# Performance work log

Measured on AMD Instinct MI355X. Metric: run time of the kernel, lower is better.

## Reference

```python
import jax, jax.numpy as jnp
import numpy as np

N, E, B = 25000, 400000, 64          # nodes, edges, graphs
F, ED, H, C = 32, 8, 4, 32           # feature/edge dims, heads, per-head dim
HC = H * C
L = 4                                # init conv + 3 stacked convs (same shapes)
LIN = 128


def setup_inputs() -> dict:
    key = jax.random.key(0)
    ks = jax.random.split(key, 24)
    s = 0.05
    inp = {
        "x": jax.random.normal(ks[0], (N, F), jnp.float32),
        "edge_attr": jax.random.normal(ks[1], (E, ED), jnp.float32),
        "edge_index": jax.random.randint(ks[2], (2, E), 0, N),
        "batch_index": jnp.sort(jax.random.randint(ks[3], (N,), 0, B)),
        # stacked TransformerConv params (leading dim = layer)
        "Wq": jax.random.normal(ks[4], (L, F, HC), jnp.float32) * s,
        "bq": jnp.zeros((L, HC), jnp.float32),
        "Wk": jax.random.normal(ks[5], (L, F, HC), jnp.float32) * s,
        "bk": jnp.zeros((L, HC), jnp.float32),
        "Wv": jax.random.normal(ks[6], (L, F, HC), jnp.float32) * s,
        "bv": jnp.zeros((L, HC), jnp.float32),
        "We": jax.random.normal(ks[7], (L, ED, HC), jnp.float32) * s,
        "be": jnp.zeros((L, HC), jnp.float32),
        "Wskip": jax.random.normal(ks[8], (L, F, HC), jnp.float32) * s,
        "bskip": jnp.zeros((L, HC), jnp.float32),
        "Wbeta": jax.random.normal(ks[9], (L, 3 * HC, 1), jnp.float32) * s,
        # per-layer Linear(H*C -> emb) + BatchNorm
        "Wlin": jax.random.normal(ks[10], (L, HC, F), jnp.float32) * s,
        "blin": jnp.zeros((L, F), jnp.float32),
        "bn_gamma": jnp.ones((L, F), jnp.float32),
        "bn_beta": jnp.zeros((L, F), jnp.float32),
        # readout MLP
        "W1": jax.random.normal(ks[11], (2 * F, LIN), jnp.float32) * s,
        "b1": jnp.zeros((LIN,), jnp.float32),
        "W2": jax.random.normal(ks[12], (LIN, LIN // 2), jnp.float32) * s,
        "b2": jnp.zeros((LIN // 2,), jnp.float32),
        "W3": jax.random.normal(ks[13], (LIN // 2, 1), jnp.float32) * s,
        "b3": jnp.zeros((1,), jnp.float32),
    }
    return inp


def _transformer_conv(x, edge_attr, src, dst, Wq, bq, Wk, bk, Wv, bv, We, be,
                      Wskip, bskip, Wbeta):
    """PyG TransformerConv(heads=H, concat=True, beta=True, edge_dim=ED), eval mode."""
    n = x.shape[0]
    q = (x @ Wq + bq).reshape(n, H, C)
    k = (x @ Wk + bk).reshape(n, H, C)
    v = (x @ Wv + bv).reshape(n, H, C)
    e = (edge_attr @ We + be).reshape(-1, H, C)          # [E,H,C]
    kj = k[src] + e                                       # key_j + edge
    alpha = jnp.einsum('ehc,ehc->eh', q[dst], kj) / np.sqrt(C).astype(np.float32)
    # segment softmax over incoming edges per destination node
    amax = jax.ops.segment_max(alpha, dst, num_segments=n)
    a = jnp.exp(alpha - amax[dst])
    denom = jax.ops.segment_sum(a, dst, num_segments=n)
    a = a / denom[dst]                                    # [E,H]
    msg = (v[src] + e) * a[:, :, None]
    out = jax.ops.segment_sum(msg, dst, num_segments=n).reshape(n, HC)
    x_skip = x @ Wskip + bskip
    beta = jax.nn.sigmoid(
        jnp.concatenate([out, x_skip, out - x_skip], axis=-1) @ Wbeta)  # [N,1]
    return beta * x_skip + (1.0 - beta) * out


def _bn(h, gamma, beta):
    m = h.mean(axis=0)
    v = h.var(axis=0)
    return (h - m) * jax.lax.rsqrt(v + 1e-5) * gamma + beta


def reference(x, edge_attr, edge_index, batch_index,
              Wq, bq, Wk, bk, Wv, bv, We, be, Wskip, bskip, Wbeta,
              Wlin, blin, bn_gamma, bn_beta, W1, b1, W2, b2, W3, b3):
    src, dst = edge_index[0], edge_index[1]
    counts = jax.ops.segment_sum(jnp.ones((N,), jnp.float32), batch_index,
                                 num_segments=B)[:, None]
    h = x
    rep = jnp.zeros((B, 2 * F), jnp.float32)
    for i in range(L):
        h = _transformer_conv(h, edge_attr, src, dst,
                              Wq[i], bq[i], Wk[i], bk[i], Wv[i], bv[i],
                              We[i], be[i], Wskip[i], bskip[i], Wbeta[i])
        h = jax.nn.elu(h @ Wlin[i] + blin[i])
        h = _bn(h, bn_gamma[i], bn_beta[i])
        if i > 0:  # original pools only inside the n_layers loop
            gmx = jax.ops.segment_max(h, batch_index, num_segments=B)
            gmean = jax.ops.segment_sum(h, batch_index, num_segments=B) / counts
            rep = rep + jnp.concatenate([gmx, gmean], axis=1)
    z = jax.nn.elu(rep @ W1 + b1)
    z = jax.nn.elu(z @ W2 + b2)
    return z @ W3 + b3  # [B,1]
```

## Files before the change

kernel.cpp:

```cpp
#include <hip/hip_runtime.h>
#include <hip/hip_bf16.h>
#include <hip/hip_fp16.h>
#include <math.h>

#define NN 25000
#define EE 400000
#define BB 64
#define FF 32
#define EDD 8
#define HH 4
#define CC 32
#define HCC 128
#define LL 4
#define LINN 128

#define RSQRT_C 0.17677669529663687f
#define NREP 16
#define NREPP 8
#define GMAX_OFF (NREP * 64)
#define GSUM_OFF (NREP * 64 + NREPP * BB * 32)
#define LSTATS_WORDS (NREP * 64 + 2 * NREPP * BB * 32)


__global__ void deg_kernel(const int* __restrict__ dst, int* __restrict__ deg) {
    int i = blockIdx.x * blockDim.x + threadIdx.x;
    if (i < EE) atomicAdd(&deg[dst[i]], 1);
}

__global__ void scan1_kernel(const int* __restrict__ deg, int* __restrict__ rowp, int* __restrict__ blks) {
    __shared__ int s[256];
    int i = blockIdx.x * 256 + threadIdx.x;
    int v = (i < NN) ? deg[i] : 0;
    s[threadIdx.x] = v;
    __syncthreads();
    for (int off = 1; off < 256; off <<= 1) {
        int t = (threadIdx.x >= off) ? s[threadIdx.x - off] : 0;
        __syncthreads();
        s[threadIdx.x] += t;
        __syncthreads();
    }
    if (i < NN) rowp[i + 1] = s[threadIdx.x];
    if (threadIdx.x == 255) blks[blockIdx.x] = s[255];
    if (i == 0) rowp[0] = 0;
}

__global__ void scan2_kernel(int* __restrict__ blks, int nb,
                             const int* __restrict__ bidx, int* __restrict__ gstart) {
    __shared__ int s[128];
    int t = threadIdx.x;
    int v = (t < nb) ? blks[t] : 0;
    s[t] = v;
    __syncthreads();
    for (int off = 1; off < 128; off <<= 1) {
        int u = (t >= off) ? s[t - off] : 0;
        __syncthreads();
        s[t] += u;
        __syncthreads();
    }
    if (t < nb) blks[t] = s[t] - v;
    if (t <= BB) {
        int lo = 0, hi = NN;
        while (lo < hi) { int mid = (lo + hi) >> 1; if (bidx[mid] < t) lo = mid + 1; else hi = mid; }
        gstart[t] = lo;
    }
}

__global__ void scan3_kernel(int* __restrict__ rowp, const int* __restrict__ blks) {
    int i = blockIdx.x * 256 + threadIdx.x;
    if (i < NN) rowp[i + 1] += blks[blockIdx.x];
}

__global__ void fill_kernel(const int* __restrict__ dst, const int* __restrict__ rowp,
                            int* __restrict__ cnt2, int* __restrict__ eid) {
    int i = blockIdx.x * blockDim.x + threadIdx.x;
    if (i < EE) {
        int d = dst[i];
        int pos = rowp[d] + atomicAdd(&cnt2[d], 1);
        eid[pos] = i;
    }
}

__global__ void sortseg_kernel(const int* __restrict__ rowp, int* __restrict__ eid) {
    int n = blockIdx.x * 256 + threadIdx.x;
    if (n >= NN) return;
    int b = rowp[n], e = rowp[n + 1];
    int d = e - b;
    if (d <= 1) return;
    if (d <= 64) {
        int buf[64];
        for (int i = 0; i < d; ++i) buf[i] = eid[b + i];
        for (int i = 1; i < d; ++i) {
            int key = buf[i];
            int j = i - 1;
            while (j >= 0 && buf[j] > key) { buf[j + 1] = buf[j]; --j; }
            buf[j + 1] = key;
        }
        for (int i = 0; i < d; ++i) eid[b + i] = buf[i];
    } else {
        for (int i = b + 1; i < e; ++i) {
            int key = eid[i];
            int j = i - 1;
            while (j >= b && eid[j] > key) { eid[j + 1] = eid[j]; --j; }
            eid[j + 1] = key;
        }
    }
}

__global__ void csr_gather_kernel(const int* __restrict__ csre, const int* __restrict__ srcA,
                                  const float* __restrict__ eattr,
                                  int* __restrict__ csrsrc, uint4* __restrict__ eh) {
    int j = blockIdx.x * blockDim.x + threadIdx.x;
    if (j < EE) {
        int e = csre[j];
        csrsrc[j] = srcA[e];
        const float4* s = (const float4*)(eattr + (size_t)e * 8);
        float4 s0 = s[0], s1 = s[1];
        __half2 h0 = __float22half2_rn(make_float2(s0.x, s0.y));
        __half2 h1 = __float22half2_rn(make_float2(s0.z, s0.w));
        __half2 h2 = __float22half2_rn(make_float2(s1.x, s1.y));
        __half2 h3 = __float22half2_rn(make_float2(s1.z, s1.w));
        uint4 o;
        o.x = *(unsigned*)&h0; o.y = *(unsigned*)&h1;
        o.z = *(unsigned*)&h2; o.w = *(unsigned*)&h3;
        eh[j] = o;
    }
}

__global__ __launch_bounds__(256) void qkvs_kernel(
    const float* __restrict__ hin, int applyBN, const float* __restrict__ bnss,
    const float* __restrict__ Wq, const float* __restrict__ bq,
    const float* __restrict__ Wk, const float* __restrict__ bk,
    const float* __restrict__ Wv, const float* __restrict__ bv,
    const float* __restrict__ Ws, const float* __restrict__ bs,
    __half2* __restrict__ qo, __half2* __restrict__ kvo,
    __half2* __restrict__ so, float* __restrict__ lstats)
{
    if (blockIdx.x == 0) {
        for (int i = threadIdx.x; i < LSTATS_WORDS; i += 256) lstats[i] = 0.0f;
    }
    __shared__ float xs[32][32];
    __shared__ float sbns[64];
    if (threadIdx.x < 64) sbns[threadIdx.x] = applyBN ? bnss[threadIdx.x] : (threadIdx.x < 32 ? 1.0f : 0.0f);
    int lane = threadIdx.x & 63;
    int sel = threadIdx.x >> 6;
    const float* W = (sel == 0) ? Wq : (sel == 1) ? Wk : (sel == 2) ? Wv : Ws;
    const float* bias = (sel == 0) ? bq : (sel == 1) ? bk : (sel == 2) ? bv : bs;
    float w0[32], w1[32];
#pragma unroll
    for (int f = 0; f < 32; ++f) {
        float2 t = *(const float2*)&W[f * 128 + 2 * lane];
        w0[f] = t.x; w1[f] = t.y;
    }
    float2 bvv = *(const float2*)&bias[2 * lane];

    int c = lane >> 1;
    int pr = lane & 1;
    int h2k = c * 4 + pr;
    int h2v = c * 4 + 2 + pr;

    for (int chunk = blockIdx.x * 32; chunk < NN; chunk += gridDim.x * 32) {
        __syncthreads();
        for (int i = threadIdx.x; i < 1024; i += 256) {
            int nn = chunk + (i >> 5);
            int ch = i & 31;
            float v = (nn < NN) ? hin[nn * 32 + ch] : 0.0f;
            xs[i >> 5][ch] = v * sbns[ch] + sbns[32 + ch];
        }
        __syncthreads();
        int nmax = NN - chunk; if (nmax > 32) nmax = 32;
        for (int nl = 0; nl < nmax; ++nl) {
            float a0 = bvv.x, a1 = bvv.y;
#pragma unroll
            for (int f = 0; f < 32; ++f) {
                float xv = xs[nl][f];
                a0 += xv * w0[f];
                a1 += xv * w1[f];
            }
            size_t node = (size_t)(chunk + nl);
            __half2 hv = __float22half2_rn(make_float2(a0, a1));
            if (sel == 0)      qo[node * 64 + lane] = hv;
            else if (sel == 1) kvo[node * 128 + h2k] = hv;
            else if (sel == 2) kvo[node * 128 + h2v] = hv;
            else               so[node * 64 + lane] = hv;
        }
    }
}

__device__ __forceinline__ unsigned fmap_u(float x) {
    unsigned u = __float_as_uint(x);
    return (u & 0x80000000u) ? ~u : (u | 0x80000000u);
}
__device__ __forceinline__ float funmap_u(unsigned u) {
    unsigned b = (u & 0x80000000u) ? (u & 0x7fffffffu) : ~u;
    return __uint_as_float(b);
}

__global__ __launch_bounds__(256) void attn_kernel(
    const uint2* __restrict__ qh, const uint4* __restrict__ kvb4,
    const uint2* __restrict__ skh,
    const uint4* __restrict__ eh,
    const int* __restrict__ srcArr,
    const int* __restrict__ rowp,
    const int* __restrict__ bidx,
    const float* __restrict__ WeL, const float* __restrict__ beL,
    const float* __restrict__ WbL,
    const float* __restrict__ WlinL, const float* __restrict__ blinL,
    float* __restrict__ hlin, float* __restrict__ lstats,
    int doPool, int doWriteH)
{
    __shared__ __align__(16) float shc[4 * 128];
    __shared__ float sbn[64];

    int tid = threadIdx.x;
    if (tid < 64) sbn[tid] = 0.0f;
    __syncthreads();

    int w = tid >> 6;
    int lane = tid & 63;
    int n = blockIdx.x * 4 + w;

    if (n < NN) {
        int c = lane & 31;
        int h = lane >> 5;

        float4 we[8];
#pragma unroll
        for (int d = 0; d < 8; ++d) we[d] = *(const float4*)&WeL[d * 128 + 4 * c];
        float4 be4 = *(const float4*)&beL[4 * c];

        uint2 qraw = qh[(size_t)n * 32 + c];
        float2 q01 = __half22float2(*(const __half2*)&qraw.x);
        float2 q23 = __half22float2(*(const __half2*)&qraw.y);
        float4 q4 = make_float4(q01.x * RSQRT_C, q01.y * RSQRT_C,
                                q23.x * RSQRT_C, q23.y * RSQRT_C);

        int beg = rowp[n], end = rowp[n + 1];
        int cnt = end - beg;
        int last = end - 1;

        float s = 0.0f, a0 = 0.0f, a1 = 0.0f, a2 = 0.0f, a3 = 0.0f;

        uint4 kvA = make_uint4(0u, 0u, 0u, 0u), kvB = kvA;
        uint4 eaA = kvA, eaB = kvA;
        int snC = 0, snD = 0;

        if (cnt > 0) {
            int j0 = beg + h;     j0 = (j0 < end) ? j0 : last;
            int j1 = beg + 2 + h; j1 = (j1 < end) ? j1 : last;
            int j2 = beg + 4 + h; j2 = (j2 < end) ? j2 : last;
            int j3 = beg + 6 + h; j3 = (j3 < end) ? j3 : last;
            int snA = srcArr[j0];
            int snB = srcArr[j1];
            snC = srcArr[j2];
            snD = srcArr[j3];
            kvA = kvb4[(size_t)snA * 32 + c];
            kvB = kvb4[(size_t)snB * 32 + c];
            eaA = eh[j0];
            eaB = eh[j1];
        }

        for (int jb = beg; jb < end; jb += 2) {
            int j = jb + h;
            uint4 kvC = kvb4[(size_t)snC * 32 + c];
            int jn = (j + 4 < end) ? j + 4 : last;
            uint4 eaC = eh[jn];
            int j8 = (j + 8 < end) ? j + 8 : last;
            int snE = srcArr[j8];

            float2 e01 = __half22float2(*(const __half2*)&eaA.x);
            float2 e23 = __half22float2(*(const __half2*)&eaA.y);
            float2 e45 = __half22float2(*(const __half2*)&eaA.z);
            float2 e67 = __half22float2(*(const __half2*)&eaA.w);
            float ead[8] = { e01.x, e01.y, e23.x, e23.y, e45.x, e45.y, e67.x, e67.y };

            float ex = be4.x, ey = be4.y, ez = be4.z, ew = be4.w;
#pragma unroll
            for (int d = 0; d < 8; ++d) {
                ex = fmaf(ead[d], we[d].x, ex);
                ey = fmaf(ead[d], we[d].y, ey);
                ez = fmaf(ead[d], we[d].z, ez);
                ew = fmaf(ead[d], we[d].w, ew);
            }

            float2 k01 = __half22float2(*(const __half2*)&kvA.x);
            float2 k23 = __half22float2(*(const __half2*)&kvA.y);
            float2 v01 = __half22float2(*(const __half2*)&kvA.z);
            float2 v23 = __half22float2(*(const __half2*)&kvA.w);

            float p = q4.x * (k01.x + ex) + q4.y * (k01.y + ey)
                    + q4.z * (k23.x + ez) + q4.w * (k23.y + ew);
            p += __shfl_xor(p, 1);
            p += __shfl_xor(p, 2);
            p += __shfl_xor(p, 4);
            float wg = (j < end) ? __expf(p) : 0.0f;
            s += wg;
            a0 = fmaf(wg, v01.x + ex, a0);
            a1 = fmaf(wg, v01.y + ey, a1);
            a2 = fmaf(wg, v23.x + ez, a2);
            a3 = fmaf(wg, v23.y + ew, a3);

            kvA = kvB; kvB = kvC;
            eaA = eaB; eaB = eaC;
            snC = snD; snD = snE;
        }

        s  += __shfl_xor(s, 32);
        a0 += __shfl_xor(a0, 32);
        a1 += __shfl_xor(a1, 32);
        a2 += __shfl_xor(a2, 32);
        a3 += __shfl_xor(a3, 32);

        float rs = (cnt > 0) ? (1.0f / s) : 0.0f;
        float o0 = a0 * rs, o1 = a1 * rs, o2 = a2 * rs, o3 = a3 * rs;

        uint2 skraw = skh[(size_t)n * 32 + c];
        float2 s01 = __half22float2(*(const __half2*)&skraw.x);
        float2 s23 = __half22float2(*(const __half2*)&skraw.y);
        float4 sk4 = make_float4(s01.x, s01.y, s23.x, s23.y);

        float4 wbo = *(const float4*)&WbL[4 * c];
        float4 wbs = *(const float4*)&WbL[128 + 4 * c];
        float4 wbd = *(const float4*)&WbL[256 + 4 * c];

        float t = o0 * wbo.x + sk4.x * wbs.x + (o0 - sk4.x) * wbd.x
                + o1 * wbo.y + sk4.y * wbs.y + (o1 - sk4.y) * wbd.y
                + o2 * wbo.z + sk4.z * wbs.z + (o2 - sk4.z) * wbd.z
                + o3 * wbo.w + sk4.w * wbs.w + (o3 - sk4.w) * wbd.w;
#pragma unroll
        for (int off = 1; off <= 16; off <<= 1) t += __shfl_xor(t, off);
        float beta = 1.0f / (1.0f + __expf(-t));
        float4 hc4;
        hc4.x = beta * sk4.x + (1.0f - beta) * o0;
        hc4.y = beta * sk4.y + (1.0f - beta) * o1;
        hc4.z = beta * sk4.z + (1.0f - beta) * o2;
        hc4.w = beta * sk4.w + (1.0f - beta) * o3;
        if (h == 0) ((float4*)shc)[w * 32 + c] = hc4;
        int cc = lane & 31;
        int half = lane >> 5;
        float acc = 0.0f;
#pragma unroll 8
        for (int i = 0; i < 64; ++i) {
            int ch = half * 64 + i;
            acc += shc[w * 128 + ch] * WlinL[ch * 32 + cc];
        }
        acc += __shfl_xor(acc, 32);
        if (lane < 32) {
            float hv = acc + blinL[lane];
            hv = (hv > 0.0f) ? hv : expm1f(hv);
            if (doWriteH) hlin[n * 32 + lane] = hv;
            atomicAdd(&sbn[lane], hv);
            atomicAdd(&sbn[32 + lane], hv * hv);
            if (doPool) {
                int g = bidx[n];
                int repv = blockIdx.x & (NREPP - 1);
                size_t idx = ((size_t)repv * BB + g) * 32 + lane;
                atomicMax((unsigned*)lstats + GMAX_OFF + idx, fmap_u(hv));
                atomicAdd(lstats + GSUM_OFF + idx, hv);
            }
        }
    }
    __syncthreads();
    if (tid < 64) atomicAdd(&lstats[(blockIdx.x & (NREP - 1)) * 64 + tid], sbn[tid]);
}

__global__ void bnfin_kernel(const float* __restrict__ bnpart,
                             const float* __restrict__ gamma, const float* __restrict__ bnbeta,
                             float* __restrict__ bnss) {
    int c = threadIdx.x;
    if (c < 32) {
        float sm = 0.0f, sq = 0.0f;
#pragma unroll
        for (int r = 0; r < NREP; ++r) { sm += bnpart[r * 64 + c]; sq += bnpart[r * 64 + 32 + c]; }
        float mean = sm * (1.0f / NN);
        float var = sq * (1.0f / NN) - mean * mean;
        float scale = gamma[c] * rsqrtf(var + 1e-5f);
        bnss[c] = scale;
        bnss[32 + c] = bnbeta[c] - mean * scale;
    }
}

__global__ void repupd_kernel(const float* __restrict__ lstats, const float* __restrict__ bnss,
                              const int* __restrict__ gstart, float* __restrict__ rep, int assign) {
    int i = blockIdx.x * blockDim.x + threadIdx.x;
    if (i < BB * 32) {
        int g = i >> 5, ch = i & 31;
        int cntg = gstart[g + 1] - gstart[g];
        float vmax = 0.0f, vmean = 0.0f;
        if (cntg > 0) {
            const unsigned* gm = (const unsigned*)lstats + GMAX_OFF;
            const float* gs = lstats + GSUM_OFF;
            unsigned mx = 0u;
            float sum = 0.0f;
#pragma unroll
            for (int r = 0; r < NREPP; ++r) {
                size_t idx = ((size_t)r * BB + g) * 32 + ch;
                unsigned m = gm[idx];
                mx = (m > mx) ? m : mx;
                sum += gs[idx];
            }
            float scale = bnss[ch], shift = bnss[32 + ch];
            vmax = scale * funmap_u(mx) + shift;
            vmean = scale * (sum / (float)cntg) + shift;
        }
        if (assign) {
            rep[g * 64 + ch] = vmax;
            rep[g * 64 + 32 + ch] = vmean;
        } else {
            rep[g * 64 + ch] += vmax;
            rep[g * 64 + 32 + ch] += vmean;
        }
    }
}

__device__ __forceinline__ float eluf(float x) { return x > 0.0f ? x : expm1f(x); }

__global__ __launch_bounds__(128) void readout_kernel(
    const float* __restrict__ rep,
    const float* __restrict__ W1, const float* __restrict__ b1,
    const float* __restrict__ W2, const float* __restrict__ b2,
    const float* __restrict__ W3, const float* __restrict__ b3,
    float* __restrict__ out)
{
    __shared__ float sr[64];
    __shared__ float sz1[128];
    __shared__ float sz2[64];
    int g = blockIdx.x;
    int t = threadIdx.x;
    if (t < 64) sr[t] = rep[g * 64 + t];
    __syncthreads();
    float acc = b1[t];
#pragma unroll 8
    for (int i = 0; i < 64; ++i) acc += sr[i] * W1[i * 128 + t];
    sz1[t] = eluf(acc);
    __syncthreads();
    if (t < 64) {
        float a2 = b2[t];
#pragma unroll 8
        for (int i = 0; i < 128; ++i) a2 += sz1[i] * W2[i * 64 + t];
        sz2[t] = eluf(a2);
    }
    __syncthreads();
    if (t < 64) {
        float p = sz2[t] * W3[t];
#pragma unroll
        for (int off = 1; off <= 32; off <<= 1) p += __shfl_xor(p, off);
        if (t == 0) out[g] = p + b3[0];
    }
}


extern "C" void kernel_launch(void* const* d_in, const int* in_sizes, int n_in,
                              void* d_out, int out_size, void* d_ws, size_t ws_size,
                              hipStream_t stream) {
    const float* x      = (const float*)d_in[0];
    const float* eattr  = (const float*)d_in[1];
    const int*   eidx   = (const int*)d_in[2];
    const int*   bidx   = (const int*)d_in[3];
    const float* Wq     = (const float*)d_in[4];
    const float* bq     = (const float*)d_in[5];
    const float* Wk     = (const float*)d_in[6];
    const float* bk     = (const float*)d_in[7];
    const float* Wv     = (const float*)d_in[8];
    const float* bv     = (const float*)d_in[9];
    const float* We     = (const float*)d_in[10];
    const float* be     = (const float*)d_in[11];
    const float* Wskip  = (const float*)d_in[12];
    const float* bskip  = (const float*)d_in[13];
    const float* Wbeta  = (const float*)d_in[14];
    const float* Wlin   = (const float*)d_in[15];
    const float* blin   = (const float*)d_in[16];
    const float* bng    = (const float*)d_in[17];
    const float* bnb    = (const float*)d_in[18];
    const float* W1     = (const float*)d_in[19];
    const float* b1     = (const float*)d_in[20];
    const float* W2     = (const float*)d_in[21];
    const float* b2     = (const float*)d_in[22];
    const float* W3     = (const float*)d_in[23];
    const float* b3     = (const float*)d_in[24];
    float* out = (float*)d_out;

    char* ws = (char*)d_ws;
    size_t off = 0;
    auto alloc = [&](size_t bytes) -> char* {
        char* p = ws + off;
        off = (off + bytes + 255) & ~(size_t)255;
        return p;
    };
    int*     rowp   = (int*)alloc((NN + 1) * 4);
    int*     degcnt = (int*)alloc(2 * NN * 4);
    int*     deg    = degcnt;
    int*     cnt2   = degcnt + NN;
    int*     csre   = (int*)alloc(EE * 4);
    int*     blks   = (int*)alloc(128 * 4);
    int*     gstart = (int*)alloc((BB + 1) * 4);
    float*   rep    = (float*)alloc(BB * 64 * 4);
    __half2* qH     = (__half2*)alloc((size_t)NN * 64 * 4);
    __half2* kvB    = (__half2*)alloc((size_t)NN * 128 * 4);
    __half2* skH    = (__half2*)alloc((size_t)NN * 64 * 4);
    float*   hlin   = (float*)alloc((size_t)NN * 32 * 4);
    float*   lstats = (float*)alloc(LSTATS_WORDS * 4);
    float*   bnss   = (float*)alloc(64 * 4);
    int*     csrsrc = (int*)alloc(EE * 4);
    uint4*   ecsrh  = (uint4*)alloc((size_t)EE * 16);

    const int* srcA = eidx;
    const int* dstA = eidx + EE;

    (void)hipMemsetAsync(degcnt, 0, 2 * NN * 4, stream);

    deg_kernel<<<(EE + 255) / 256, 256, 0, stream>>>(dstA, deg);
    scan1_kernel<<<98, 256, 0, stream>>>(deg, rowp, blks);
    scan2_kernel<<<1, 128, 0, stream>>>(blks, 98, bidx, gstart);
    scan3_kernel<<<98, 256, 0, stream>>>(rowp, blks);
    fill_kernel<<<(EE + 255) / 256, 256, 0, stream>>>(dstA, rowp, cnt2, csre);
    sortseg_kernel<<<98, 256, 0, stream>>>(rowp, csre);
    csr_gather_kernel<<<(EE + 255) / 256, 256, 0, stream>>>(csre, srcA, eattr, csrsrc, ecsrh);

    const float* hin = x;
    for (int l = 0; l < LL; ++l) {
        qkvs_kernel<<<782, 256, 0, stream>>>(
            (l == 0) ? x : hlin, (l > 0) ? 1 : 0, bnss,
            Wq + l * FF * HCC, bq + l * HCC,
            Wk + l * FF * HCC, bk + l * HCC,
            Wv + l * FF * HCC, bv + l * HCC,
            Wskip + l * FF * HCC, bskip + l * HCC,
            qH, kvB, skH, lstats);

        attn_kernel<<<(NN + 3) / 4, 256, 0, stream>>>(
            (const uint2*)qH, (const uint4*)kvB, (const uint2*)skH,
            ecsrh, csrsrc, rowp, bidx,
            We + l * EDD * HCC, be + l * HCC,
            Wbeta + l * 3 * HCC,
            Wlin + l * HCC * FF, blin + l * FF,
            hlin, lstats,
            (l > 0) ? 1 : 0, (l < LL - 1) ? 1 : 0);

        bnfin_kernel<<<1, 32, 0, stream>>>(lstats, bng + l * FF, bnb + l * FF, bnss);

        if (l > 0) {
            repupd_kernel<<<8, 256, 0, stream>>>(lstats, bnss, gstart, rep, (l == 1) ? 1 : 0);
        }
        hin = hlin;
    }

    readout_kernel<<<64, 128, 0, stream>>>(rep, W1, b1, W2, b2, W3, b3, out);
}
```

Measured before the change: 541.2 us.

## Fold BN finalize into qkvs and repupd kernels, double-buffer stats

```diff
diff --git a/kernel.cpp b/kernel.cpp
--- a/kernel.cpp
+++ b/kernel.cpp
@@ -127,20 +127,38 @@
 }
 
 __global__ __launch_bounds__(256) void qkvs_kernel(
-    const float* __restrict__ hin, int applyBN, const float* __restrict__ bnss,
+    const float* __restrict__ hin, int applyBN,
+    const float* __restrict__ lstats_prev, float* __restrict__ lstats_cur,
+    const float* __restrict__ gamma, const float* __restrict__ bnbeta,
     const float* __restrict__ Wq, const float* __restrict__ bq,
     const float* __restrict__ Wk, const float* __restrict__ bk,
     const float* __restrict__ Wv, const float* __restrict__ bv,
     const float* __restrict__ Ws, const float* __restrict__ bs,
     __half2* __restrict__ qo, __half2* __restrict__ kvo,
-    __half2* __restrict__ so, float* __restrict__ lstats)
+    __half2* __restrict__ so)
 {
     if (blockIdx.x == 0) {
-        for (int i = threadIdx.x; i < LSTATS_WORDS; i += 256) lstats[i] = 0.0f;
+        for (int i = threadIdx.x; i < LSTATS_WORDS; i += 256) lstats_cur[i] = 0.0f;
     }
     __shared__ float xs[32][32];
     __shared__ float sbns[64];
-    if (threadIdx.x < 64) sbns[threadIdx.x] = applyBN ? bnss[threadIdx.x] : (threadIdx.x < 32 ? 1.0f : 0.0f);
+    if (threadIdx.x < 32) {
+        float scale = 1.0f, shift = 0.0f;
+        if (applyBN) {
+            float sm = 0.0f, sq = 0.0f;
+#pragma unroll
+            for (int r = 0; r < NREP; ++r) {
+                sm += lstats_prev[r * 64 + threadIdx.x];
+                sq += lstats_prev[r * 64 + 32 + threadIdx.x];
+            }
+            float mean = sm * (1.0f / NN);
+            float var = sq * (1.0f / NN) - mean * mean;
+            scale = gamma[threadIdx.x] * rsqrtf(var + 1e-5f);
+            shift = bnbeta[threadIdx.x] - mean * scale;
+        }
+        sbns[threadIdx.x] = scale;
+        sbns[32 + threadIdx.x] = shift;
+    }
     int lane = threadIdx.x & 63;
     int sel = threadIdx.x >> 6;
     const float* W = (sel == 0) ? Wq : (sel == 1) ? Wk : (sel == 2) ? Wv : Ws;
@@ -171,10 +189,16 @@
         for (int nl = 0; nl < nmax; ++nl) {
             float a0 = bvv.x, a1 = bvv.y;
 #pragma unroll
-            for (int f = 0; f < 32; ++f) {
-                float xv = xs[nl][f];
-                a0 += xv * w0[f];
-                a1 += xv * w1[f];
+            for (int f4 = 0; f4 < 8; ++f4) {
+                float4 xv = *(const float4*)&xs[nl][f4 * 4];
+                a0 = fmaf(xv.x, w0[f4 * 4],     a0);
+                a1 = fmaf(xv.x, w1[f4 * 4],     a1);
+                a0 = fmaf(xv.y, w0[f4 * 4 + 1], a0);
+                a1 = fmaf(xv.y, w1[f4 * 4 + 1], a1);
+                a0 = fmaf(xv.z, w0[f4 * 4 + 2], a0);
+                a1 = fmaf(xv.z, w1[f4 * 4 + 2], a1);
+                a0 = fmaf(xv.w, w0[f4 * 4 + 3], a0);
+                a1 = fmaf(xv.w, w1[f4 * 4 + 3], a1);
             }
             size_t node = (size_t)(chunk + nl);
             __half2 hv = __float22half2_rn(make_float2(a0, a1));
@@ -195,7 +219,7 @@
     return __uint_as_float(b);
 }
 
-__global__ __launch_bounds__(256) void attn_kernel(
+__global__ __launch_bounds__(256, 8) void attn_kernel(
     const uint2* __restrict__ qh, const uint4* __restrict__ kvb4,
     const uint2* __restrict__ skh,
     const uint4* __restrict__ eh,
@@ -363,27 +387,20 @@
     if (tid < 64) atomicAdd(&lstats[(blockIdx.x & (NREP - 1)) * 64 + tid], sbn[tid]);
 }
 
-__global__ void bnfin_kernel(const float* __restrict__ bnpart,
-                             const float* __restrict__ gamma, const float* __restrict__ bnbeta,
-                             float* __restrict__ bnss) {
-    int c = threadIdx.x;
-    if (c < 32) {
-        float sm = 0.0f, sq = 0.0f;
-#pragma unroll
-        for (int r = 0; r < NREP; ++r) { sm += bnpart[r * 64 + c]; sq += bnpart[r * 64 + 32 + c]; }
-        float mean = sm * (1.0f / NN);
-        float var = sq * (1.0f / NN) - mean * mean;
-        float scale = gamma[c] * rsqrtf(var + 1e-5f);
-        bnss[c] = scale;
-        bnss[32 + c] = bnbeta[c] - mean * scale;
-    }
-}
-
-__global__ void repupd_kernel(const float* __restrict__ lstats, const float* __restrict__ bnss,
+__global__ void repupd_kernel(const float* __restrict__ lstats,
+                              const float* __restrict__ gamma, const float* __restrict__ bnbeta,
                               const int* __restrict__ gstart, float* __restrict__ rep, int assign) {
     int i = blockIdx.x * blockDim.x + threadIdx.x;
     if (i < BB * 32) {
         int g = i >> 5, ch = i & 31;
+        float sm = 0.0f, sq = 0.0f;
+#pragma unroll
+        for (int r = 0; r < NREP; ++r) { sm += lstats[r * 64 + ch]; sq += lstats[r * 64 + 32 + ch]; }
+        float mean = sm * (1.0f / NN);
+        float var = sq * (1.0f / NN) - mean * mean;
+        float scale = gamma[ch] * rsqrtf(var + 1e-5f);
+        float shift = bnbeta[ch] - mean * scale;
+
         int cntg = gstart[g + 1] - gstart[g];
         float vmax = 0.0f, vmean = 0.0f;
         if (cntg > 0) {
@@ -398,7 +415,6 @@
                 mx = (m > mx) ? m : mx;
                 sum += gs[idx];
             }
-            float scale = bnss[ch], shift = bnss[32 + ch];
             vmax = scale * funmap_u(mx) + shift;
             vmean = scale * (sum / (float)cntg) + shift;
         }
@@ -498,8 +514,7 @@
     __half2* kvB    = (__half2*)alloc((size_t)NN * 128 * 4);
     __half2* skH    = (__half2*)alloc((size_t)NN * 64 * 4);
     float*   hlin   = (float*)alloc((size_t)NN * 32 * 4);
-    float*   lstats = (float*)alloc(LSTATS_WORDS * 4);
-    float*   bnss   = (float*)alloc(64 * 4);
+    float*   lstats = (float*)alloc(2 * LSTATS_WORDS * 4);
     int*     csrsrc = (int*)alloc(EE * 4);
     uint4*   ecsrh  = (uint4*)alloc((size_t)EE * 16);
 
@@ -516,15 +531,19 @@
     sortseg_kernel<<<98, 256, 0, stream>>>(rowp, csre);
     csr_gather_kernel<<<(EE + 255) / 256, 256, 0, stream>>>(csre, srcA, eattr, csrsrc, ecsrh);
 
-    const float* hin = x;
     for (int l = 0; l < LL; ++l) {
+        float* lcur = lstats + (size_t)(l & 1) * LSTATS_WORDS;
+        float* lprev = lstats + (size_t)((l & 1) ^ 1) * LSTATS_WORDS;
+
         qkvs_kernel<<<782, 256, 0, stream>>>(
-            (l == 0) ? x : hlin, (l > 0) ? 1 : 0, bnss,
+            (l == 0) ? x : hlin, (l > 0) ? 1 : 0,
+            lprev, lcur,
+            bng + (l > 0 ? (l - 1) : 0) * FF, bnb + (l > 0 ? (l - 1) : 0) * FF,
             Wq + l * FF * HCC, bq + l * HCC,
             Wk + l * FF * HCC, bk + l * HCC,
             Wv + l * FF * HCC, bv + l * HCC,
             Wskip + l * FF * HCC, bskip + l * HCC,
-            qH, kvB, skH, lstats);
+            qH, kvB, skH);
 
         attn_kernel<<<(NN + 3) / 4, 256, 0, stream>>>(
             (const uint2*)qH, (const uint4*)kvB, (const uint2*)skH,
@@ -532,15 +551,13 @@
             We + l * EDD * HCC, be + l * HCC,
             Wbeta + l * 3 * HCC,
             Wlin + l * HCC * FF, blin + l * FF,
-            hlin, lstats,
+            hlin, lcur,
             (l > 0) ? 1 : 0, (l < LL - 1) ? 1 : 0);
 
-        bnfin_kernel<<<1, 32, 0, stream>>>(lstats, bng + l * FF, bnb + l * FF, bnss);
-
         if (l > 0) {
-            repupd_kernel<<<8, 256, 0, stream>>>(lstats, bnss, gstart, rep, (l == 1) ? 1 : 0);
-        }
-        hin = hlin;
+            repupd_kernel<<<8, 256, 0, stream>>>(lcur, bng + l * FF, bnb + l * FF,
+                                                 gstart, rep, (l == 1) ? 1 : 0);
+        }
     }
 
     readout_kernel<<<64, 128, 0, stream>>>(rep, W1, b1, W2, b2, W3, b3, out);
```

Measured after the change: 1.370 ms. 153% more time.
